# Kernel optimization log

Measured on AMD Instinct MI355X. Metric: run time of the kernel, lower is better.

## Reference

```python
import jax, jax.numpy as jnp
import numpy as np

H = 12          # heads (longformer-base)
DH = 64         # head dim
W = 256         # one-sided window (attention_window=512 in HF convention)


def _heads(t, B, S):
    return t.reshape(B, S, H, DH).transpose(0, 2, 1, 3)  # [B,H,S,dh]


def _forward(x, mask, clss, emb, pos, wq, wk, wv, wo, wqg, wkg, wvg):
    B, S = x.shape
    D = emb.shape[1]
    h = emb[x] + pos[None, :S]                      # [B,S,D]

    scale = DH ** -0.5
    q = _heads(h @ wq, B, S) * scale                # [B,H,S,dh]
    k = _heads(h @ wk, B, S)
    v = _heads(h @ wv, B, S)

    # ---- sliding-window (banded) attention, chunked like HF ----
    nc = S // W
    kpos = (jnp.arange(nc) * W - W)[:, None] + jnp.arange(3 * W)[None, :]   # [nc,3w] absolute key pos
    kidx = kpos + W                                  # index into padded seq
    kp = jnp.pad(k, ((0, 0), (0, 0), (W, W), (0, 0)))
    vp = jnp.pad(v, ((0, 0), (0, 0), (W, W), (0, 0)))
    Kc = kp[:, :, kidx, :]                           # [B,H,nc,3w,dh]
    Vc = vp[:, :, kidx, :]
    Qc = q.reshape(B, H, nc, W, DH)
    band = jnp.einsum('bhcqd,bhckd->bhcqk', Qc, Kc)  # [B,H,nc,w,3w]

    qpos = (jnp.arange(nc) * W)[:, None] + jnp.arange(W)[None, :]           # [nc,w]
    rel = kpos[:, None, :] - qpos[:, :, None]                               # [nc,w,3w]
    inband = (rel >= -W) & (rel <= W) & (kpos[:, None, :] >= 0) & (kpos[:, None, :] < S)

    is_global = jnp.zeros((S,), bool).at[clss].set(True)
    kpos_c = jnp.clip(kpos, 0, S - 1)
    # global keys are handled via dedicated columns, so remove them from the band (as HF does)
    key_ok = (mask[:, kpos_c] != 0) & (~is_global[kpos_c])                  # [B,nc,3w]

    NEG = jnp.finfo(band.dtype).min
    m = inband[None, None] & key_ok[:, None, :, None, :]                    # [B,H,nc,w,3w]
    band = jnp.where(m, band, NEG)
    band_flat = band.reshape(B, H, S, 3 * W)

    # ---- local queries attending to global keys ----
    kg_loc = k[:, :, clss, :]                        # [B,H,G,dh]
    vg_loc = v[:, :, clss, :]
    sg = jnp.einsum('bhsd,bhgd->bhsg', q, kg_loc)
    gm = (mask[:, clss] != 0)[:, None, None, :]
    sg = jnp.where(gm, sg, NEG)

    scores = jnp.concatenate([band_flat, sg], axis=-1)   # [B,H,S,3w+G]
    probs = jax.nn.softmax(scores, axis=-1)
    p_band = probs[..., : 3 * W].reshape(B, H, nc, W, 3 * W)
    p_g = probs[..., 3 * W:]
    out = jnp.einsum('bhcqk,bhckd->bhcqd', p_band, Vc).reshape(B, H, S, DH)
    out = out + jnp.einsum('bhsg,bhgd->bhsd', p_g, vg_loc)

    # ---- global queries: full attention with separate global projections ----
    qg = _heads(h @ wqg, B, S)[:, :, clss, :] * scale    # [B,H,G,dh]
    kg = _heads(h @ wkg, B, S)
    vg = _heads(h @ wvg, B, S)
    sgg = jnp.einsum('bhgd,bhsd->bhgs', qg, kg)
    sgg = jnp.where((mask != 0)[:, None, None, :], sgg, NEG)
    og = jnp.einsum('bhgs,bhsd->bhgd', jax.nn.softmax(sgg, axis=-1), vg)
    out = out.at[:, :, clss, :].set(og)

    top_vec = out.transpose(0, 2, 1, 3).reshape(B, S, D) @ wo
    return top_vec


def setup_inputs() -> dict:
    key = jax.random.key(0)
    ks = jax.random.split(key, 12)
    B, S, D, V, G = 2, 4096, 768, 50265, 64
    std = 0.02
    x = jax.random.randint(ks[0], (B, S), 0, V)
    mask = jnp.ones((B, S), jnp.int32)
    clss = jnp.sort(jax.random.randint(ks[1], (G,), 0, S))
    emb = jax.random.normal(ks[2], (V, D), jnp.float32) * std
    pos = jax.random.normal(ks[3], (S, D), jnp.float32) * std
    wq = jax.random.normal(ks[4], (D, D), jnp.float32) * std
    wk = jax.random.normal(ks[5], (D, D), jnp.float32) * std
    wv = jax.random.normal(ks[6], (D, D), jnp.float32) * std
    wo = jax.random.normal(ks[7], (D, D), jnp.float32) * std
    wqg = jax.random.normal(ks[8], (D, D), jnp.float32) * std
    wkg = jax.random.normal(ks[9], (D, D), jnp.float32) * std
    wvg = jax.random.normal(ks[10], (D, D), jnp.float32) * std
    return {"x": x, "mask": mask, "clss": clss, "emb": emb, "pos": pos,
            "wq": wq, "wk": wk, "wv": wv, "wo": wo,
            "wqg": wqg, "wkg": wkg, "wvg": wvg}


def reference(x, mask, clss, emb, pos, wq, wk, wv, wo, wqg, wkg, wvg):
    return _forward(x, mask, clss, emb, pos, wq, wk, wv, wo, wqg, wkg, wvg)
```

## Files before the change

kernel.cpp:

```cpp
#include <hip/hip_runtime.h>
#include <stdint.h>

typedef unsigned short u16;
typedef unsigned char u8;
typedef unsigned int u32;
typedef __attribute__((ext_vector_type(8))) short short8x;
typedef __attribute__((ext_vector_type(4))) float f32x4;
typedef __attribute__((ext_vector_type(16))) float f32x16;

#define DEV static __device__ __forceinline__

DEV u16 f2bf(float f) {
  union { float f; unsigned u; } v; v.f = f;
  unsigned r = v.u + 0x7FFFu + ((v.u >> 16) & 1u);
  return (u16)(r >> 16);
}
DEV int imin(int a, int b) { return a < b ? a : b; }
DEV int imax(int a, int b) { return a > b ? a : b; }
DEV float ex2(float x) { return __builtin_exp2f(x); }

DEV void gload16(const void* g, void* l) {
  __builtin_amdgcn_global_load_lds((const __attribute__((address_space(1))) void*)g,
                                   (__attribute__((address_space(3))) void*)l, 16, 0, 0);
}

DEV u32 cvtpk_bf16(float lo, float hi) {
  u32 r;
  asm("v_cvt_pk_bf16_f32 %0, %1, %2" : "=v"(r) : "v"(lo), "v"(hi));
  return r;
}
DEV void plswap(u32& a, u32& b) {
  asm("v_permlane32_swap_b32 %0, %1" : "+v"(a), "+v"(b));
}

#define LOG2E 1.44269504f

struct WPtrs { const float* p[7]; };

__global__ __launch_bounds__(256) void prep_kernel(
    WPtrs wp, const int* __restrict__ x, const float* __restrict__ emb,
    const float* __restrict__ pos, const int* __restrict__ clss,
    const int* __restrict__ mask, u16* __restrict__ wt, u16* __restrict__ hb,
    u16* __restrict__ hg, u32* __restrict__ kv32, u32* __restrict__ mv32,
    u32* __restrict__ mc32) {
  __shared__ __align__(16) char smraw[64 * 72 * 4];
  const int bid = blockIdx.x;
  const int t = threadIdx.x;

  if (bid < 1008) {
    const int mat = bid / 144;
    const int inner = bid - mat * 144;
    const int kt = inner % 12, nt = inner / 12;
    const float* __restrict__ w = wp.p[mat];
    float(*tile)[72] = (float(*)[72])smraw;
    {
      const int kk = t >> 2, n0 = (t & 3) * 16;
      const float* src = w + (size_t)(kt * 64 + kk) * 768 + nt * 64 + n0;
#pragma unroll
      for (int i = 0; i < 4; ++i)
        *(float4*)&tile[kk][n0 + i * 4] = *(const float4*)(src + i * 4);
    }
    __syncthreads();
    {
      const int nn = t >> 2, k0 = (t & 3) * 16;
      u16* dst = wt + (size_t)(mat * 768 + nt * 64 + nn) * 768 + kt * 64 + k0;
      short8x v0, v1;
#pragma unroll
      for (int j = 0; j < 8; ++j) {
        v0[j] = (short)f2bf(tile[k0 + j][nn]);
        v1[j] = (short)f2bf(tile[k0 + 8 + j][nn]);
      }
      *(short8x*)dst = v0;
      *(short8x*)(dst + 8) = v1;
    }
    return;
  }
  if (bid < 2032) {
    const int vb = bid - 1008;
    const int n4 = 2 * 4096 * 192;
    for (int i = vb * 256 + t; i < n4; i += 1024 * 256) {
      const int r = i / 192;
      const int d4 = i - r * 192;
      const int s = r & 4095;
      const int tok = x[r];
      const float4 e = *(const float4*)(emb + (size_t)tok * 768 + d4 * 4);
      const float4 p = *(const float4*)(pos + (size_t)s * 768 + d4 * 4);
      union { u16 u[4]; uint2 v; } o;
      o.u[0] = f2bf(e.x + p.x);
      o.u[1] = f2bf(e.y + p.y);
      o.u[2] = f2bf(e.z + p.z);
      o.u[3] = f2bf(e.w + p.w);
      *(uint2*)(hb + (size_t)r * 768 + d4 * 4) = o.v;
    }
    return;
  }
  if (bid == 2032) {
    u8* isg = (u8*)smraw;
    for (int i = t; i < 4096; i += 256) isg[i] = 0;
    __syncthreads();
    if (t < 64) isg[clss[t]] = 1;
    __syncthreads();
    {
      const int b = t >> 7, i = t & 127;
      u32 kv = 0, mvv = 0;
      for (int j = 0; j < 32; ++j) {
        const int key = i * 32 + j;
        const u32 m = (u32)(mask[b * 4096 + key] != 0);
        mvv |= m << j;
        kv |= (m & (u32)(isg[key] == 0)) << j;
      }
      kv32[b * 128 + i] = kv;
      mv32[b * 128 + i] = mvv;
    }
    if (t < 4) {
      const int b = t >> 1, wi = t & 1;
      u32 mc = 0;
      for (int j = 0; j < 32; ++j) {
        const int g = wi * 32 + j;
        mc |= (u32)(mask[b * 4096 + clss[g]] != 0) << j;
      }
      mc32[b * 2 + wi] = mc;
    }
    return;
  }
  {
    const int i = (bid - 2033) * 256 + t;
    const int r = i / 192, d4 = i - r * 192;
    const int b = r >> 6, g = r & 63;
    const int s = clss[g];
    const int tok = x[b * 4096 + s];
    const float4 e = *(const float4*)(emb + (size_t)tok * 768 + d4 * 4);
    const float4 p = *(const float4*)(pos + (size_t)s * 768 + d4 * 4);
    union { u16 u[4]; uint2 v; } o;
    o.u[0] = f2bf(e.x + p.x);
    o.u[1] = f2bf(e.y + p.y);
    o.u[2] = f2bf(e.z + p.z);
    o.u[3] = f2bf(e.w + p.w);
    *(uint2*)(hg + (size_t)r * 768 + d4 * 4) = o.v;
  }
}

struct Outs6 { u16* p[6]; };

template <int MODE>
__global__ __launch_bounds__(256) void gemm_kernel(const u16* __restrict__ A, const u16* __restrict__ Bt,
                                                   const u16* __restrict__ A2, const u16* __restrict__ Bt2,
                                                   Outs6 outs, float* __restrict__ outF) {
  __shared__ __align__(16) u16 smA[2][128 * 64];
  __shared__ __align__(16) u16 smB[2][128 * 64];
  const int t = threadIdx.x;
  const int l = t & 63, w = t >> 6;
  const int l15 = l & 15, grp = l >> 4;
  const int wm = w >> 1, wn = w & 1;
  int bx, by;
  bool qg = false;
  if (MODE == 0) {
    int id = blockIdx.x;
    if (id >= 1920) {
      qg = true;
      bx = id - 1920;
      by = 0;
    } else {
      const int xcd = id & 7;
      const int j = id >> 3;
      by = xcd * 8 + (j & 7);
      bx = j >> 3;
    }
  } else {
    const int xcd = blockIdx.x & 7;
    const int j = blockIdx.x >> 3;
    by = xcd * 8 + (j & 7);
    bx = j >> 3;
  }
  const u16* __restrict__ Ap = (MODE == 0 && qg) ? A2 : A;
  const u16* __restrict__ Btp = (MODE == 0 && qg) ? Bt2 : Bt;
  const int m0 = by * 128, n0 = bx * 128;
  const f32x4 zero4 = {0.f, 0.f, 0.f, 0.f};
  f32x4 acc[4][4];
#pragma unroll
  for (int mi = 0; mi < 4; ++mi)
#pragma unroll
    for (int ni = 0; ni < 4; ++ni) acc[mi][ni] = zero4;

  const int sr = l >> 3;
  const int ssl = ((l & 7) ^ sr) << 4;

  auto STAGE = [&](int kb, int d) {
#pragma unroll
    for (int c = 0; c < 4; ++c) {
      const int rg = w * 4 + c;
      const int r = rg * 8 + sr;
      gload16(Ap + (size_t)(m0 + r) * 768 + kb * 64 + (ssl >> 1), (char*)smA[d] + rg * 1024);
      gload16(Btp + (size_t)(n0 + r) * 768 + kb * 64 + (ssl >> 1), (char*)smB[d] + rg * 1024);
    }
  };
  const int xorf = (l15 & 7) << 4;
  auto RDA = [&](int d, int mi, int kk) {
    return *(const short8x*)((const char*)smA[d] + (wm * 64 + mi * 16 + l15) * 128 + ((kk * 64 + grp * 16) ^ xorf));
  };
  auto RDB = [&](int d, int ni, int kk) {
    return *(const short8x*)((const char*)smB[d] + (wn * 64 + ni * 16 + l15) * 128 + ((kk * 64 + grp * 16) ^ xorf));
  };

  STAGE(0, 0);
  STAGE(1, 1);
  asm volatile("s_waitcnt vmcnt(8)" ::: "memory");
  __builtin_amdgcn_s_barrier();
  __builtin_amdgcn_sched_barrier(0);

  short8x a0[4], b0[4], a1[4], b1[4];
#pragma unroll
  for (int i = 0; i < 4; ++i) { a0[i] = RDA(0, i, 0); b0[i] = RDB(0, i, 0); }

  for (int kt = 0; kt < 12; ++kt) {
    const int cur = kt & 1;
#pragma unroll
    for (int i = 0; i < 4; ++i) { a1[i] = RDA(cur, i, 1); b1[i] = RDB(cur, i, 1); }
    __builtin_amdgcn_s_setprio(1);
#pragma unroll
    for (int mi = 0; mi < 4; ++mi)
#pragma unroll
      for (int ni = 0; ni < 4; ++ni)
        acc[mi][ni] = __builtin_amdgcn_mfma_f32_16x16x32_bf16(a0[mi], b0[ni], acc[mi][ni], 0, 0, 0);
    __builtin_amdgcn_s_setprio(0);
    if (kt < 11) {
      asm volatile("s_waitcnt lgkmcnt(0)" ::: "memory");
      __builtin_amdgcn_s_barrier();
      __builtin_amdgcn_sched_barrier(0);
      if (kt < 10) {
        STAGE(kt + 2, cur);
        asm volatile("s_waitcnt vmcnt(8)" ::: "memory");
      } else {
        asm volatile("s_waitcnt vmcnt(0)" ::: "memory");
      }
      __builtin_amdgcn_s_barrier();
      __builtin_amdgcn_sched_barrier(0);
#pragma unroll
      for (int i = 0; i < 4; ++i) { a0[i] = RDA(cur ^ 1, i, 0); b0[i] = RDB(cur ^ 1, i, 0); }
    }
    __builtin_amdgcn_s_setprio(1);
#pragma unroll
    for (int mi = 0; mi < 4; ++mi)
#pragma unroll
      for (int ni = 0; ni < 4; ++ni)
        acc[mi][ni] = __builtin_amdgcn_mfma_f32_16x16x32_bf16(a1[mi], b1[ni], acc[mi][ni], 0, 0, 0);
    __builtin_amdgcn_s_setprio(0);
  }

  if (MODE == 0) {
    if (qg) {
      u16* __restrict__ base = outs.p[5];
#pragma unroll
      for (int mi = 0; mi < 4; ++mi)
#pragma unroll
        for (int ni = 0; ni < 4; ++ni) {
          const int col = n0 + wn * 64 + ni * 16 + l15;
          const int hd = col >> 6, dh = col & 63;
#pragma unroll
          for (int rr = 0; rr < 4; ++rr) {
            const int row = wm * 64 + mi * 16 + grp * 4 + rr;
            const int b = row >> 6, g = row & 63;
            base[((size_t)(b * 12 + hd) * 64 + g) * 64 + dh] = f2bf(acc[mi][ni][rr] * 0.125f * LOG2E);
          }
        }
      return;
    }
    const int mat = bx / 6;
    const int inn0 = n0 - mat * 768 + wn * 64;
    u16* __restrict__ base = outs.p[mat];
    if (mat == 2 || mat == 4) {
#pragma unroll
      for (int mi = 0; mi < 4; ++mi) {
        const int row0 = m0 + wm * 64 + mi * 16 + grp * 4;
        const int b = row0 >> 12, s = row0 & 4095;
#pragma unroll
        for (int ni = 0; ni < 4; ++ni) {
          const int col = inn0 + ni * 16 + l15;
          const int hd = col >> 6, dh = col & 63;
          union { u16 u[4]; uint2 v; } o;
#pragma unroll
          for (int rr = 0; rr < 4; ++rr) o.u[rr] = f2bf(acc[mi][ni][rr]);
          *(uint2*)(base + ((size_t)(b * 12 + hd) * 64 + dh) * 4096 + s) = o.v;
        }
      }
    } else {
      const float scl = (mat == 0) ? 0.125f * LOG2E : 1.0f;
#pragma unroll
      for (int mi = 0; mi < 4; ++mi)
#pragma unroll
        for (int ni = 0; ni < 4; ++ni) {
          const int col = inn0 + ni * 16 + l15;
          const int hd = col >> 6, dh = col & 63;
#pragma unroll
          for (int rr = 0; rr < 4; ++rr) {
            const int row = m0 + wm * 64 + mi * 16 + grp * 4 + rr;
            const int b = row >> 12, s = row & 4095;
            base[((size_t)(b * 12 + hd) * 4096 + s) * 64 + dh] = f2bf(acc[mi][ni][rr] * scl);
          }
        }
    }
  } else {
#pragma unroll
    for (int mi = 0; mi < 4; ++mi)
#pragma unroll
      for (int rr = 0; rr < 4; ++rr) {
        const int row = m0 + wm * 64 + mi * 16 + grp * 4 + rr;
#pragma unroll
        for (int ni = 0; ni < 4; ++ni) {
          const int col = n0 + wn * 64 + ni * 16 + l15;
          outF[(size_t)row * 768 + col] = acc[mi][ni][rr];
        }
      }
  }
}

__global__ __launch_bounds__(256) void gcls_kernel(const u16* __restrict__ kB, const u16* __restrict__ vTs,
                                                   const int* __restrict__ clss,
                                                   u16* __restrict__ kcls, u16* __restrict__ vtcls) {
  const int bh = blockIdx.x;
  __shared__ int sc[64];
  const int t = threadIdx.x;
  if (t < 64) sc[t] = clss[t];
  __syncthreads();
  {
    const int g = t >> 2, d0 = (t & 3) * 16;
    const int row = sc[g];
    const u16* pk = kB + ((size_t)bh * 4096 + row) * 64 + d0;
    u16* ok = kcls + ((size_t)bh * 64 + g) * 64 + d0;
    *(short8x*)ok = *(const short8x*)pk;
    *(short8x*)(ok + 8) = *(const short8x*)(pk + 8);
  }
  {
    const int dh = t >> 2, g0 = (t & 3) * 16;
    const u16* vrow = vTs + ((size_t)bh * 64 + dh) * 4096;
    short8x v0, v1;
#pragma unroll
    for (int j = 0; j < 8; ++j) {
      v0[j] = (short)vrow[sc[g0 + j]];
      v1[j] = (short)vrow[sc[g0 + 8 + j]];
    }
    u16* o = vtcls + ((size_t)bh * 64 + dh) * 64 + g0;
    *(short8x*)o = v0;
    *(short8x*)(o + 8) = v1;
  }
}

struct AttnState {
  f32x16 a0, a1;
  float m, l;
};

#define ATTN_SOFTMAX_PV(S, s0, s1, vm0, vm1, LOADV0, LOADV1)                        \
  {                                                                                  \
    float mx[8];                                                                     \
    _Pragma("unroll") for (int e = 0; e < 8; ++e)                                    \
        mx[e] = fmaxf(fmaxf(s0[e], s0[e + 8]), fmaxf(s1[e], s1[e + 8]));             \
    mx[0] = fmaxf(mx[0], mx[4]); mx[1] = fmaxf(mx[1], mx[5]);                        \
    mx[2] = fmaxf(mx[2], mx[6]); mx[3] = fmaxf(mx[3], mx[7]);                        \
    mx[0] = fmaxf(mx[0], mx[2]); mx[1] = fmaxf(mx[1], mx[3]);                        \
    float mv = fmaxf(mx[0], mx[1]);                                                  \
    mv = fmaxf(mv, __shfl_xor(mv, 32));                                              \
    if (!__all(mv <= S.m + 8.f)) {                                                   \
      const float mn = fmaxf(S.m, mv);                                               \
      const float sc = ex2(S.m - mn);                                                \
      S.m = mn; S.l *= sc;                                                           \
      _Pragma("unroll") for (int e = 0; e < 16; ++e) { S.a0[e] *= sc; S.a1[e] *= sc; } \
    }                                                                                \
    float p0[16], p1[16];                                                            \
    if ((vm0 & vm1) == 0xFFFFFFFFu) {                                                \
      _Pragma("unroll") for (int e = 0; e < 16; ++e) {                               \
        p0[e] = ex2(s0[e] - S.m); p1[e] = ex2(s1[e] - S.m);                          \
      }                                                                              \
    } else {                                                                         \
      const u32 w0 = vm0 >> (hf * 4), w1 = vm1 >> (hf * 4);                          \
      _Pragma("unroll") for (int e = 0; e < 16; ++e) {                               \
        const int cr = (e & 3) + 8 * (e >> 2);                                       \
        p0[e] = ex2(s0[e] - S.m) * (float)((w0 >> cr) & 1u);                         \
        p1[e] = ex2(s1[e] - S.m) * (float)((w1 >> cr) & 1u);                         \
      }                                                                              \
    }                                                                                \
    float sm[8];                                                                     \
    _Pragma("unroll") for (int e = 0; e < 8; ++e)                                    \
        sm[e] = (p0[e] + p0[e + 8]) + (p1[e] + p1[e + 8]);                           \
    sm[0] += sm[4]; sm[1] += sm[5]; sm[2] += sm[6]; sm[3] += sm[7];                  \
    sm[0] += sm[2]; sm[1] += sm[3];                                                  \
    float ls = sm[0] + sm[1];                                                        \
    ls += __shfl_xor(ls, 32);                                                        \
    S.l += ls;                                                                       \
    _Pragma("unroll") for (int st = 0; st < 2; ++st) {                               \
      const float* pp = st ? p1 : p0;                                                \
      _Pragma("unroll") for (int c = 0; c < 2; ++c) {                                \
        u32 A1 = cvtpk_bf16(pp[8 * c + 0], pp[8 * c + 1]);                           \
        u32 A2 = cvtpk_bf16(pp[8 * c + 2], pp[8 * c + 3]);                           \
        u32 B1 = cvtpk_bf16(pp[8 * c + 4], pp[8 * c + 5]);                           \
        u32 B2 = cvtpk_bf16(pp[8 * c + 6], pp[8 * c + 7]);                           \
        plswap(A1, B1); plswap(A2, B2);                                              \
        union { u32 w[4]; short8x v; } u;                                            \
        u.w[0] = A1; u.w[1] = A2; u.w[2] = B1; u.w[3] = B2;                          \
        const int sc4 = st * 2 + c;                                                  \
        const short8x vf0 = LOADV0(sc4);                                             \
        const short8x vf1 = LOADV1(sc4);                                             \
        S.a0 = __builtin_amdgcn_mfma_f32_32x32x16_bf16(vf0, u.v, S.a0, 0, 0, 0);     \
        S.a1 = __builtin_amdgcn_mfma_f32_32x32x16_bf16(vf1, u.v, S.a1, 0, 0, 0);     \
      }                                                                              \
    }                                                                                \
  }

DEV void attn_tile64(const u16* __restrict__ kp, const u16* __restrict__ vp, int vstr,
                     u32 vm0, u32 vm1, const short8x* qf, AttnState& S, int l31, int hf) {
  const int h8 = hf * 8;
  const f32x16 z16 = {0.f};
  f32x16 s0 = z16, s1 = z16;
  const u16* kr0 = kp + (size_t)l31 * 64 + h8;
  const u16* kr1 = kr0 + 32 * 64;
#pragma unroll
  for (int ks = 0; ks < 4; ++ks) {
    const short8x kf0 = *(const short8x*)(kr0 + ks * 16);
    const short8x kf1 = *(const short8x*)(kr1 + ks * 16);
    s0 = __builtin_amdgcn_mfma_f32_32x32x16_bf16(kf0, qf[ks], s0, 0, 0, 0);
    s1 = __builtin_amdgcn_mfma_f32_32x32x16_bf16(kf1, qf[ks], s1, 0, 0, 0);
  }
#define LV0(sc4) (*(const short8x*)(vp + (sc4) * 16 + h8 + (size_t)l31 * vstr))
#define LV1(sc4) (*(const short8x*)(vp + (sc4) * 16 + h8 + (size_t)(32 + l31) * vstr))
  ATTN_SOFTMAX_PV(S, s0, s1, vm0, vm1, LV0, LV1)
#undef LV0
#undef LV1
}

DEV void attn_tile64_lds(const char* __restrict__ Kl, const char* __restrict__ Vl,
                         u32 vm0, u32 vm1, const short8x* qf, AttnState& S, int l31, int hf) {
  const int swz = (l31 & 7) << 4;
  const f32x16 z16 = {0.f};
  f32x16 s0 = z16, s1 = z16;
#pragma unroll
  for (int ks = 0; ks < 4; ++ks) {
    const int cb = (hf * 16 + ks * 32) ^ swz;
    const short8x kf0 = *(const short8x*)(Kl + l31 * 128 + cb);
    const short8x kf1 = *(const short8x*)(Kl + (32 + l31) * 128 + cb);
    s0 = __builtin_amdgcn_mfma_f32_32x32x16_bf16(kf0, qf[ks], s0, 0, 0, 0);
    s1 = __builtin_amdgcn_mfma_f32_32x32x16_bf16(kf1, qf[ks], s1, 0, 0, 0);
  }
#define LV0(sc4) (*(const short8x*)(Vl + l31 * 128 + (((sc4) * 32 + hf * 16) ^ swz)))
#define LV1(sc4) (*(const short8x*)(Vl + (32 + l31) * 128 + (((sc4) * 32 + hf * 16) ^ swz)))
  ATTN_SOFTMAX_PV(S, s0, s1, vm0, vm1, LV0, LV1)
#undef LV0
#undef LV1
}

DEV u32 bandmask32(int q, int kb2) {
  const int lo = imax(q - 256 - kb2, 0);
  const int hi = imin(q + 256 - kb2, 31);
  if (hi < lo) return 0u;
  return (0xFFFFFFFFu << lo) & (0xFFFFFFFFu >> (31 - hi));
}

struct FusedArgs {
  const u16 *qB, *kB, *vT, *kcls, *vtcls, *qgc, *kgB, *vgT;
  const u32 *kv32, *mv32, *mc32;
  u16* aout;
  float *pm, *pl, *pacc;
};

__global__ __launch_bounds__(256, 3) void band_kernel(FusedArgs a) {
  const int t = threadIdx.x;
  const int w = t >> 6, l = t & 63;
  const int l31 = l & 31, hf = l >> 5, h4 = hf * 4;
  const f32x16 z16 = {0.f};

  __shared__ __align__(16) char Ktile[2][8192];
  __shared__ __align__(16) char Vtile[2][8192];

  if (blockIdx.x < 96) {
    const int wid = blockIdx.x * 4 + w;
    const int sl = wid & 7;
    const int qsub = (wid >> 3) & 1;
    const int bh = wid >> 4;
    const int b = bh / 12;
    const int q = qsub * 32 + l31;

    const u16* kgb = a.kgB + (size_t)bh * 4096 * 64;
    const u16* vgb = a.vgT + (size_t)bh * 64 * 4096;
    short8x qf[4];
#pragma unroll
    for (int ks = 0; ks < 4; ++ks)
      qf[ks] = *(const short8x*)(a.qgc + ((size_t)bh * 64 + q) * 64 + ks * 16 + hf * 8);

    AttnState S;
    S.a0 = z16; S.a1 = z16; S.m = -60.f; S.l = 0.f;
    for (int tt = sl * 8; tt < sl * 8 + 8; ++tt) {
      const int kb = tt * 64;
      const u32 vm0 = a.mv32[b * 128 + tt * 2];
      const u32 vm1 = a.mv32[b * 128 + tt * 2 + 1];
      attn_tile64(kgb + (size_t)kb * 64, vgb + kb, 4096, vm0, vm1, qf, S, l31, hf);
    }
    const int pbase = (bh * 8 + sl) * 64;
    float* pr = a.pacc + ((size_t)pbase + q) * 64;
#pragma unroll
    for (int rq = 0; rq < 4; ++rq) {
      f32x4 v0 = {S.a0[rq * 4 + 0], S.a0[rq * 4 + 1], S.a0[rq * 4 + 2], S.a0[rq * 4 + 3]};
      f32x4 v1 = {S.a1[rq * 4 + 0], S.a1[rq * 4 + 1], S.a1[rq * 4 + 2], S.a1[rq * 4 + 3]};
      *(f32x4*)(pr + rq * 8 + h4) = v0;
      *(f32x4*)(pr + 32 + rq * 8 + h4) = v1;
    }
    if (hf == 0) {
      a.pm[pbase + q] = S.m;
      a.pl[pbase + q] = S.l;
    }
    return;
  }

  int bid = blockIdx.x - 96;
  bid = (bid & 7) * 96 + (bid >> 3);
  const int qblk = bid & 31;
  const int h = (bid >> 5) % 12;
  const int b = bid / 384;
  const int bh = b * 12 + h;
  const int q0b = qblk * 128;
  const int q0w = q0b + w * 32;
  const int q = q0w + l31;

  const u16* kbh = a.kB + (size_t)bh * 4096 * 64;
  const u16* vbh = a.vT + (size_t)bh * 64 * 4096;
  const u16* kcb = a.kcls + (size_t)bh * 4096;
  const u16* vcb = a.vtcls + (size_t)bh * 4096;

  short8x qf[4];
#pragma unroll
  for (int ks = 0; ks < 4; ++ks)
    qf[ks] = *(const short8x*)(a.qB + ((size_t)bh * 4096 + q) * 64 + ks * 16 + hf * 8);

  AttnState S;
  S.a0 = z16; S.a1 = z16; S.m = -60.f; S.l = 0.f;

  const int tloB = imax(0, q0b - 256) >> 6;
  const int thiB = imin(63, (q0b + 383) >> 6);
  const int nB = thiB - tloB + 1;
  const int tlo_w = (imax(0, q0w - 256) >> 6) - tloB;
  const int thi_w = (imin(63, (q0w + 287) >> 6)) - tloB;

  auto STAGEi = [&](int j, int buf) {
    const u16* ksrc;
    const u16* vsrc;
    int vstr;
    if (j == nB) { ksrc = kcb; vsrc = vcb; vstr = 64; }
    else {
      ksrc = kbh + (size_t)(tloB + j) * 64 * 64;
      vsrc = vbh + (size_t)(tloB + j) * 64;
      vstr = 4096;
    }
#pragma unroll
    for (int c = 0; c < 2; ++c) {
      const int rw = w + 4 * c;
      const int row = rw * 8 + (l >> 3);
      const int seg = (l & 7) ^ (row & 7);
      gload16(ksrc + (size_t)row * 64 + seg * 8, Ktile[buf] + rw * 1024);
      gload16(vsrc + (size_t)row * vstr + seg * 8, Vtile[buf] + rw * 1024);
    }
  };

  STAGEi(0, 0);
  STAGEi(1, 1);
  asm volatile("s_waitcnt vmcnt(4)" ::: "memory");
  __builtin_amdgcn_s_barrier();
  __builtin_amdgcn_sched_barrier(0);

  for (int i = 0; i <= nB; ++i) {
    const int buf = i & 1;
    const bool isG = (i == nB);
    if (isG || (i >= tlo_w && i <= thi_w)) {
      u32 vm0, vm1;
      if (isG) {
        vm0 = a.mc32[b * 2];
        vm1 = a.mc32[b * 2 + 1];
      } else {
        const int tt = tloB + i;
        const int kb = tt * 64;
        vm0 = a.kv32[b * 128 + tt * 2];
        vm1 = a.kv32[b * 128 + tt * 2 + 1];
        const int d0 = kb - q0w, d1 = kb + 32 - q0w;
        if (d0 < -225 || d0 > 225) vm0 &= bandmask32(q, kb);
        if (d1 < -225 || d1 > 225) vm1 &= bandmask32(q, kb + 32);
      }
      attn_tile64_lds(Ktile[buf], Vtile[buf], vm0, vm1, qf, S, l31, hf);
    }
    if (i < nB) {
      asm volatile("s_waitcnt lgkmcnt(0)" ::: "memory");
      __builtin_amdgcn_s_barrier();
      __builtin_amdgcn_sched_barrier(0);
      if (i + 2 <= nB) {
        STAGEi(i + 2, buf);
        asm volatile("s_waitcnt vmcnt(4)" ::: "memory");
      } else {
        asm volatile("s_waitcnt vmcnt(0)" ::: "memory");
      }
      __builtin_amdgcn_s_barrier();
      __builtin_amdgcn_sched_barrier(0);
    }
  }

  const float inv = 1.f / S.l;
  u16* ob = a.aout + ((size_t)b * 4096 + q) * 768 + h * 64;
#pragma unroll
  for (int rq = 0; rq < 4; ++rq) {
    union { u16 s[4]; uint2 v; } o0, o1;
#pragma unroll
    for (int j = 0; j < 4; ++j) {
      o0.s[j] = f2bf(S.a0[rq * 4 + j] * inv);
      o1.s[j] = f2bf(S.a1[rq * 4 + j] * inv);
    }
    *(uint2*)(ob + rq * 8 + h4) = o0.v;
    *(uint2*)(ob + 32 + rq * 8 + h4) = o1.v;
  }
}

__global__ __launch_bounds__(256) void ogm_kernel(const float* __restrict__ pm, const float* __restrict__ pl,
                                                  const float* __restrict__ pacc, const int* __restrict__ clss,
                                                  u16* __restrict__ aout) {
  const int bh = blockIdx.x;
  const int b = bh / 12, h = bh % 12;
  const int t = threadIdx.x;
  const int r = t >> 2, cs = (t & 3) * 16;
  float mv[8];
  float M = -1e30f;
#pragma unroll
  for (int s = 0; s < 8; ++s) {
    mv[s] = pm[(bh * 8 + s) * 64 + r];
    M = fmaxf(M, mv[s]);
  }
  float L = 0.f, f[8];
#pragma unroll
  for (int s = 0; s < 8; ++s) {
    f[s] = ex2(mv[s] - M);
    L += pl[(bh * 8 + s) * 64 + r] * f[s];
  }
  float o[16];
#pragma unroll
  for (int j = 0; j < 16; ++j) o[j] = 0.f;
#pragma unroll
  for (int s = 0; s < 8; ++s) {
    const float* pr = pacc + (size_t)(bh * 8 + s) * 4096 + r * 64 + cs;
#pragma unroll
    for (int j4 = 0; j4 < 4; ++j4) {
      const float4 a = *(const float4*)(pr + j4 * 4);
      o[j4 * 4 + 0] += a.x * f[s];
      o[j4 * 4 + 1] += a.y * f[s];
      o[j4 * 4 + 2] += a.z * f[s];
      o[j4 * 4 + 3] += a.w * f[s];
    }
  }
  const float inv = 1.f / L;
  short8x v0, v1;
#pragma unroll
  for (int j = 0; j < 8; ++j) {
    v0[j] = (short)f2bf(o[j] * inv);
    v1[j] = (short)f2bf(o[8 + j] * inv);
  }
  u16* op = aout + ((size_t)b * 4096 + clss[r]) * 768 + h * 64 + cs;
  *(short8x*)op = v0;
  *(short8x*)(op + 8) = v1;
}

extern "C" void kernel_launch(void* const* d_in, const int* in_sizes, int n_in,
                              void* d_out, int out_size, void* d_ws, size_t ws_size,
                              hipStream_t stream) {
  (void)in_sizes; (void)n_in; (void)out_size; (void)ws_size;
  const int* x = (const int*)d_in[0];
  const int* mask = (const int*)d_in[1];
  const int* clss = (const int*)d_in[2];
  const float* emb = (const float*)d_in[3];
  const float* pos = (const float*)d_in[4];
  const float* wq = (const float*)d_in[5];
  const float* wk = (const float*)d_in[6];
  const float* wv = (const float*)d_in[7];
  const float* wo = (const float*)d_in[8];
  const float* wqg = (const float*)d_in[9];
  const float* wkg = (const float*)d_in[10];
  const float* wvg = (const float*)d_in[11];
  float* out = (float*)d_out;

  char* ws = (char*)d_ws;
  size_t off = 0;
  auto alloc = [&](size_t n) { char* p = ws + off; off = (off + n + 255) & ~(size_t)255; return p; };
  const size_t SZ = (size_t)2 * 12 * 4096 * 64 * 2;
  u16* hb = (u16*)alloc(SZ);
  u16* wt = (u16*)alloc((size_t)7 * 768 * 768 * 2);
  u16* qb = (u16*)alloc(SZ);
  u16* kb = (u16*)alloc(SZ);
  u16* kgb = (u16*)alloc(SZ);
  u16* vts = (u16*)alloc(SZ);
  u16* vgts = (u16*)alloc(SZ);
  u16* hg = (u16*)alloc((size_t)128 * 768 * 2);
  u16* qgc = (u16*)alloc((size_t)24 * 64 * 64 * 2);
  u16* kcls = (u16*)alloc((size_t)24 * 64 * 64 * 2);
  u16* vtcls = (u16*)alloc((size_t)24 * 64 * 64 * 2);
  u32* kv32 = (u32*)alloc(256 * 4);
  u32* mv32 = (u32*)alloc(256 * 4);
  u32* mc32 = (u32*)alloc(4 * 4);
  u16* aout = (u16*)alloc(SZ);
  float* pm = (float*)alloc((size_t)192 * 64 * 4);
  float* pl = (float*)alloc((size_t)192 * 64 * 4);
  float* pacc = (float*)alloc((size_t)192 * 4096 * 4);

  WPtrs wp;
  wp.p[0] = wq; wp.p[1] = wk; wp.p[2] = wv; wp.p[3] = wkg; wp.p[4] = wvg; wp.p[5] = wqg; wp.p[6] = wo;

  prep_kernel<<<2129, 256, 0, stream>>>(wp, x, emb, pos, clss, mask, wt, hb, hg, kv32, mv32, mc32);

  Outs6 o5;
  o5.p[0] = qb; o5.p[1] = kb; o5.p[2] = vts; o5.p[3] = kgb; o5.p[4] = vgts; o5.p[5] = qgc;
  gemm_kernel<0><<<1926, 256, 0, stream>>>(hb, wt, hg, wt + (size_t)5 * 768 * 768, o5, nullptr);

  gcls_kernel<<<24, 256, 0, stream>>>(kb, vts, clss, kcls, vtcls);

  FusedArgs fa;
  fa.qB = qb; fa.kB = kb; fa.vT = vts; fa.kcls = kcls; fa.vtcls = vtcls;
  fa.qgc = qgc; fa.kgB = kgb; fa.vgT = vgts;
  fa.kv32 = kv32; fa.mv32 = mv32; fa.mc32 = mc32;
  fa.aout = aout; fa.pm = pm; fa.pl = pl; fa.pacc = pacc;
  band_kernel<<<864, 256, 0, stream>>>(fa);

  ogm_kernel<<<24, 256, 0, stream>>>(pm, pl, pacc, clss, aout);

  Outs6 dummy = {};
  gemm_kernel<1><<<384, 256, 0, stream>>>(aout, wt + (size_t)6 * 768 * 768, nullptr, nullptr, dummy, out);
}
```

Before: 161.2 us.

## Use 256x256 tiles with 512 threads for the fused QKV projection GEMM

Replaces the 128x128-tile projection GEMM, which ran 1920 blocks, with a new 256x256-tile kernel of 8 waves (480 blocks) to raise arithmetic intensity and reduce global/LDS traffic per FLOP. The small global-query projection, previously folded into the same launch, is split into its own 6-block launch. Larger tiles use 128KB LDS and more accumulator registers per thread, which lowers occupancy and adds a launch.

```diff
diff --git a/kernel.cpp b/kernel.cpp
--- a/kernel.cpp
+++ b/kernel.cpp
@@ -142,9 +142,133 @@
 
 struct Outs6 { u16* p[6]; };
 
+__global__ __launch_bounds__(512, 2) void gemm256_kernel(const u16* __restrict__ A, const u16* __restrict__ Bt,
+                                                         Outs6 outs) {
+  __shared__ __align__(16) u16 smA[2][256 * 64];
+  __shared__ __align__(16) u16 smB[2][256 * 64];
+  const int t = threadIdx.x;
+  const int l = t & 63, w = t >> 6;
+  const int l15 = l & 15, grp = l >> 4;
+  const int wm = w >> 2, wn = w & 3;
+  const int id = blockIdx.x;
+  const int xcd = id & 7;
+  const int j = id >> 3;
+  const int by = xcd * 4 + (j & 3);
+  const int bx = j >> 2;
+  const int m0 = by * 256, n0 = bx * 256;
+  const f32x4 zero4 = {0.f, 0.f, 0.f, 0.f};
+  f32x4 acc[8][4];
+#pragma unroll
+  for (int mi = 0; mi < 8; ++mi)
+#pragma unroll
+    for (int ni = 0; ni < 4; ++ni) acc[mi][ni] = zero4;
+
+  const int sr = l >> 3;
+  const int ssl = ((l & 7) ^ sr) << 4;
+
+  auto STAGE = [&](int kb, int d) {
+#pragma unroll
+    for (int c = 0; c < 4; ++c) {
+      const int rg = w * 4 + c;
+      const int r = rg * 8 + sr;
+      gload16(A + (size_t)(m0 + r) * 768 + kb * 64 + (ssl >> 1), (char*)smA[d] + rg * 1024);
+      gload16(Bt + (size_t)(n0 + r) * 768 + kb * 64 + (ssl >> 1), (char*)smB[d] + rg * 1024);
+    }
+  };
+  const int xorf = (l15 & 7) << 4;
+  auto RDA = [&](int d, int mi, int kk) {
+    return *(const short8x*)((const char*)smA[d] + (wm * 128 + mi * 16 + l15) * 128 + ((kk * 64 + grp * 16) ^ xorf));
+  };
+  auto RDB = [&](int d, int ni, int kk) {
+    return *(const short8x*)((const char*)smB[d] + (wn * 64 + ni * 16 + l15) * 128 + ((kk * 64 + grp * 16) ^ xorf));
+  };
+
+  STAGE(0, 0);
+  STAGE(1, 1);
+  asm volatile("s_waitcnt vmcnt(8)" ::: "memory");
+  __builtin_amdgcn_s_barrier();
+  __builtin_amdgcn_sched_barrier(0);
+
+  for (int kt = 0; kt < 12; ++kt) {
+    const int cur = kt & 1;
+    short8x bf[4][2], af[4][2];
+#pragma unroll
+    for (int ni = 0; ni < 4; ++ni) { bf[ni][0] = RDB(cur, ni, 0); bf[ni][1] = RDB(cur, ni, 1); }
+#pragma unroll
+    for (int mi = 0; mi < 4; ++mi) { af[mi][0] = RDA(cur, mi, 0); af[mi][1] = RDA(cur, mi, 1); }
+    __builtin_amdgcn_s_setprio(1);
+#pragma unroll
+    for (int mi = 0; mi < 4; ++mi)
+#pragma unroll
+      for (int ni = 0; ni < 4; ++ni) {
+        acc[mi][ni] = __builtin_amdgcn_mfma_f32_16x16x32_bf16(af[mi][0], bf[ni][0], acc[mi][ni], 0, 0, 0);
+        acc[mi][ni] = __builtin_amdgcn_mfma_f32_16x16x32_bf16(af[mi][1], bf[ni][1], acc[mi][ni], 0, 0, 0);
+      }
+    __builtin_amdgcn_s_setprio(0);
+#pragma unroll
+    for (int mi = 0; mi < 4; ++mi) { af[mi][0] = RDA(cur, mi + 4, 0); af[mi][1] = RDA(cur, mi + 4, 1); }
+    __builtin_amdgcn_s_setprio(1);
+#pragma unroll
+    for (int mi = 0; mi < 4; ++mi)
+#pragma unroll
+      for (int ni = 0; ni < 4; ++ni) {
+        acc[mi + 4][ni] = __builtin_amdgcn_mfma_f32_16x16x32_bf16(af[mi][0], bf[ni][0], acc[mi + 4][ni], 0, 0, 0);
+        acc[mi + 4][ni] = __builtin_amdgcn_mfma_f32_16x16x32_bf16(af[mi][1], bf[ni][1], acc[mi + 4][ni], 0, 0, 0);
+      }
+    __builtin_amdgcn_s_setprio(0);
+    if (kt < 11) {
+      asm volatile("s_waitcnt lgkmcnt(0)" ::: "memory");
+      __builtin_amdgcn_s_barrier();
+      __builtin_amdgcn_sched_barrier(0);
+      if (kt < 10) {
+        STAGE(kt + 2, cur);
+        asm volatile("s_waitcnt vmcnt(8)" ::: "memory");
+      } else {
+        asm volatile("s_waitcnt vmcnt(0)" ::: "memory");
+      }
+      __builtin_amdgcn_s_barrier();
+      __builtin_amdgcn_sched_barrier(0);
+    }
+  }
+
+  const int mat = bx / 3;
+  const int inn0 = n0 - mat * 768 + wn * 64;
+  u16* __restrict__ base = outs.p[mat];
+  if (mat == 2 || mat == 4) {
+#pragma unroll
+    for (int mi = 0; mi < 8; ++mi) {
+      const int row0 = m0 + wm * 128 + mi * 16 + grp * 4;
+      const int b = row0 >> 12, s = row0 & 4095;
+#pragma unroll
+      for (int ni = 0; ni < 4; ++ni) {
+        const int col = inn0 + ni * 16 + l15;
+        const int hd = col >> 6, dh = col & 63;
+        union { u16 u[4]; uint2 v; } o;
+#pragma unroll
+        for (int rr = 0; rr < 4; ++rr) o.u[rr] = f2bf(acc[mi][ni][rr]);
+        *(uint2*)(base + ((size_t)(b * 12 + hd) * 64 + dh) * 4096 + s) = o.v;
+      }
+    }
+  } else {
+    const float scl = (mat == 0) ? 0.125f * LOG2E : 1.0f;
+#pragma unroll
+    for (int mi = 0; mi < 8; ++mi)
+#pragma unroll
+      for (int ni = 0; ni < 4; ++ni) {
+        const int col = inn0 + ni * 16 + l15;
+        const int hd = col >> 6, dh = col & 63;
+#pragma unroll
+        for (int rr = 0; rr < 4; ++rr) {
+          const int row = m0 + wm * 128 + mi * 16 + grp * 4 + rr;
+          const int b = row >> 12, s = row & 4095;
+          base[((size_t)(b * 12 + hd) * 4096 + s) * 64 + dh] = f2bf(acc[mi][ni][rr] * scl);
+        }
+      }
+  }
+}
+
 template <int MODE>
 __global__ __launch_bounds__(256) void gemm_kernel(const u16* __restrict__ A, const u16* __restrict__ Bt,
-                                                   const u16* __restrict__ A2, const u16* __restrict__ Bt2,
                                                    Outs6 outs, float* __restrict__ outF) {
   __shared__ __align__(16) u16 smA[2][128 * 64];
   __shared__ __align__(16) u16 smB[2][128 * 64];
@@ -153,27 +277,15 @@
   const int l15 = l & 15, grp = l >> 4;
   const int wm = w >> 1, wn = w & 1;
   int bx, by;
-  bool qg = false;
-  if (MODE == 0) {
-    int id = blockIdx.x;
-    if (id >= 1920) {
-      qg = true;
-      bx = id - 1920;
-      by = 0;
-    } else {
-      const int xcd = id & 7;
-      const int j = id >> 3;
-      by = xcd * 8 + (j & 7);
-      bx = j >> 3;
-    }
-  } else {
+  if (MODE == 1) {
     const int xcd = blockIdx.x & 7;
     const int j = blockIdx.x >> 3;
     by = xcd * 8 + (j & 7);
     bx = j >> 3;
-  }
-  const u16* __restrict__ Ap = (MODE == 0 && qg) ? A2 : A;
-  const u16* __restrict__ Btp = (MODE == 0 && qg) ? Bt2 : Bt;
+  } else {
+    bx = blockIdx.x;
+    by = 0;
+  }
   const int m0 = by * 128, n0 = bx * 128;
   const f32x4 zero4 = {0.f, 0.f, 0.f, 0.f};
   f32x4 acc[4][4];
@@ -190,8 +302,8 @@
     for (int c = 0; c < 4; ++c) {
       const int rg = w * 4 + c;
       const int r = rg * 8 + sr;
-      gload16(Ap + (size_t)(m0 + r) * 768 + kb * 64 + (ssl >> 1), (char*)smA[d] + rg * 1024);
-      gload16(Btp + (size_t)(n0 + r) * 768 + kb * 64 + (ssl >> 1), (char*)smB[d] + rg * 1024);
+      gload16(A + (size_t)(m0 + r) * 768 + kb * 64 + (ssl >> 1), (char*)smA[d] + rg * 1024);
+      gload16(Bt + (size_t)(n0 + r) * 768 + kb * 64 + (ssl >> 1), (char*)smB[d] + rg * 1024);
     }
   };
   const int xorf = (l15 & 7) << 4;
@@ -247,58 +359,21 @@
     __builtin_amdgcn_s_setprio(0);
   }
 
-  if (MODE == 0) {
-    if (qg) {
-      u16* __restrict__ base = outs.p[5];
-#pragma unroll
-      for (int mi = 0; mi < 4; ++mi)
-#pragma unroll
-        for (int ni = 0; ni < 4; ++ni) {
-          const int col = n0 + wn * 64 + ni * 16 + l15;
-          const int hd = col >> 6, dh = col & 63;
-#pragma unroll
-          for (int rr = 0; rr < 4; ++rr) {
-            const int row = wm * 64 + mi * 16 + grp * 4 + rr;
-            const int b = row >> 6, g = row & 63;
-            base[((size_t)(b * 12 + hd) * 64 + g) * 64 + dh] = f2bf(acc[mi][ni][rr] * 0.125f * LOG2E);
-          }
+  if (MODE == 2) {
+    u16* __restrict__ base = outs.p[5];
+#pragma unroll
+    for (int mi = 0; mi < 4; ++mi)
+#pragma unroll
+      for (int ni = 0; ni < 4; ++ni) {
+        const int col = n0 + wn * 64 + ni * 16 + l15;
+        const int hd = col >> 6, dh = col & 63;
+#pragma unroll
+        for (int rr = 0; rr < 4; ++rr) {
+          const int row = wm * 64 + mi * 16 + grp * 4 + rr;
+          const int b = row >> 6, g = row & 63;
+          base[((size_t)(b * 12 + hd) * 64 + g) * 64 + dh] = f2bf(acc[mi][ni][rr] * 0.125f * LOG2E);
         }
-      return;
-    }
-    const int mat = bx / 6;
-    const int inn0 = n0 - mat * 768 + wn * 64;
-    u16* __restrict__ base = outs.p[mat];
-    if (mat == 2 || mat == 4) {
-#pragma unroll
-      for (int mi = 0; mi < 4; ++mi) {
-        const int row0 = m0 + wm * 64 + mi * 16 + grp * 4;
-        const int b = row0 >> 12, s = row0 & 4095;
-#pragma unroll
-        for (int ni = 0; ni < 4; ++ni) {
-          const int col = inn0 + ni * 16 + l15;
-          const int hd = col >> 6, dh = col & 63;
-          union { u16 u[4]; uint2 v; } o;
-#pragma unroll
-          for (int rr = 0; rr < 4; ++rr) o.u[rr] = f2bf(acc[mi][ni][rr]);
-          *(uint2*)(base + ((size_t)(b * 12 + hd) * 64 + dh) * 4096 + s) = o.v;
-        }
-      }
-    } else {
-      const float scl = (mat == 0) ? 0.125f * LOG2E : 1.0f;
-#pragma unroll
-      for (int mi = 0; mi < 4; ++mi)
-#pragma unroll
-        for (int ni = 0; ni < 4; ++ni) {
-          const int col = inn0 + ni * 16 + l15;
-          const int hd = col >> 6, dh = col & 63;
-#pragma unroll
-          for (int rr = 0; rr < 4; ++rr) {
-            const int row = m0 + wm * 64 + mi * 16 + grp * 4 + rr;
-            const int b = row >> 12, s = row & 4095;
-            base[((size_t)(b * 12 + hd) * 4096 + s) * 64 + dh] = f2bf(acc[mi][ni][rr] * scl);
-          }
-        }
-    }
+      }
   } else {
 #pragma unroll
     for (int mi = 0; mi < 4; ++mi)
@@ -708,7 +783,8 @@
 
   Outs6 o5;
   o5.p[0] = qb; o5.p[1] = kb; o5.p[2] = vts; o5.p[3] = kgb; o5.p[4] = vgts; o5.p[5] = qgc;
-  gemm_kernel<0><<<1926, 256, 0, stream>>>(hb, wt, hg, wt + (size_t)5 * 768 * 768, o5, nullptr);
+  gemm256_kernel<<<480, 512, 0, stream>>>(hb, wt, o5);
+  gemm_kernel<2><<<6, 256, 0, stream>>>(hg, wt + (size_t)5 * 768 * 768, o5, nullptr);
 
   gcls_kernel<<<24, 256, 0, stream>>>(kb, vts, clss, kcls, vtcls);
 
@@ -722,5 +798,5 @@
   ogm_kernel<<<24, 256, 0, stream>>>(pm, pl, pacc, clss, aout);
 
   Outs6 dummy = {};
-  gemm_kernel<1><<<384, 256, 0, stream>>>(aout, wt + (size_t)6 * 768 * 768, nullptr, nullptr, dummy, out);
-}
+  gemm_kernel<1><<<384, 256, 0, stream>>>(aout, wt + (size_t)6 * 768 * 768, dummy, out);
+}
```

Result: slower. 174.7 us (+8.4%).
